# Kernel tuning notes

Hardware: AMD Instinct MI355X
Metric: run time of the kernel (lower is better)

The kernel has to match this reference:

```python
import jax, jax.numpy as jnp
import numpy as np

C = 64
SHIFT = 3
NEIGHBOR_SIZES = (3, 5, 7)  # dilation = 1 for all levels
NUM_GROUPS = 8


def conv2d(x, w, b, padding=0, groups=1):
    out = jax.lax.conv_general_dilated(
        x, w, (1, 1), [(padding, padding), (padding, padding)],
        dimension_numbers=('NCHW', 'OIHW', 'NCHW'),
        feature_group_count=groups)
    return out + b[None, :, None, None]


def natten_level(q, k, v, rpb, ks):
    # q,k,v: (B,H,W,C) channels-last; rpb: (2ks-1, 2ks-1); dilation=1.
    # NATTEN semantics: window of size ks x ks centered at each query, clamped
    # (shifted) at image borders so it always lies fully inside the image.
    B, H, W, Cc = q.shape
    r = ks // 2
    i = jnp.arange(H); ni = jnp.clip(i - r, 0, H - ks)   # window row starts
    j = jnp.arange(W); nj = jnp.clip(j - r, 0, W - ks)   # window col starts
    ar = jnp.arange(ks)
    ii = ni[:, None] + ar[None, :]                        # (H,ks) neighbor rows
    jj = nj[:, None] + ar[None, :]                        # (W,ks) neighbor cols
    kn = k[:, ii][:, :, :, jj]                            # (B,H,ks,W,ks,C)
    attn = jnp.einsum('bhwc,bhpwqc->bhwpq', q, kn)        # (B,H,W,ks,ks)
    # relative-position-bias lookup: row start pi = (ks-1) + ni - i
    pi = (ks - 1) + ni - i                                # (H,)
    pj = (ks - 1) + nj - j                                # (W,)
    bias = rpb[(pi[:, None] + ar[None, :])[:, None, :, None],
               (pj[:, None] + ar[None, :])[None, :, None, :]]  # (H,W,ks,ks)
    attn = attn + bias[None]
    attn = jax.nn.softmax(attn.reshape(B, H, W, ks * ks), axis=-1)
    attn = attn.reshape(B, H, W, ks, ks)
    vn = v[:, ii][:, :, :, jj]                            # (B,H,ks,W,ks,C)
    return jnp.einsum('bhwpq,bhpwqc->bhwc', attn, vn)


def _forward(sup_frame, key_frame, conv_smooth_w, conv_smooth_b,
             conv_reduce_w, conv_reduce_b, v_w0, v_b0, v_w1, v_b1,
             v_w2, v_b2, rpb0, rpb1, rpb2, fusion_w, fusion_b):
    p = SHIFT
    outs = [sup_frame]  # original (pre-shift) support features
    # shift-roll spatial correlation
    shifts = [(sh, sw) for sh in (-p, 0, p) for sw in (-p, 0, p)
              if not (sh == 0 and sw == 0)]
    padded = jnp.pad(sup_frame, ((0, 0), (0, 0), (p, p), (p, p)))
    parts = jnp.split(padded, NUM_GROUPS, axis=1)
    shifted = jnp.concatenate(
        [jnp.roll(parts[g], shifts[g], axis=(2, 3)) for g in range(NUM_GROUPS)],
        axis=1)[..., p:-p, p:-p]
    shifted = conv2d(shifted, conv_smooth_w, conv_smooth_b, padding=1,
                     groups=NUM_GROUPS)
    sup2 = conv2d(jnp.concatenate([sup_frame, shifted], axis=1),
                  conv_reduce_w, conv_reduce_b)
    # multi-scale neighborhood attention (single head)
    q = jnp.transpose(key_frame, (0, 2, 3, 1))
    k = jnp.transpose(sup2, (0, 2, 3, 1))
    v_ws = (v_w0, v_w1, v_w2); v_bs = (v_b0, v_b1, v_b2)
    rpbs = (rpb0, rpb1, rpb2)
    for lvl, ks in enumerate(NEIGHBOR_SIZES):
        v = jnp.transpose(conv2d(sup2, v_ws[lvl], v_bs[lvl]), (0, 2, 3, 1))
        agg = natten_level(q, k, v, rpbs[lvl], ks)
        outs.append(jnp.transpose(agg, (0, 3, 1, 2)))
    fused = jnp.concatenate(outs, axis=1)  # (B, 4*C, H, W)
    return jax.nn.relu(conv2d(fused, fusion_w, fusion_b, padding=1))


def setup_inputs() -> dict:
    key = jax.random.key(0)
    ks = jax.random.split(key, 20)
    B, H, W = 4, 96, 96
    s = 0.05
    d = {}
    d['sup_frame'] = jax.random.normal(ks[0], (B, C, H, W), jnp.float32)
    d['key_frame'] = jax.random.normal(ks[1], (B, C, H, W), jnp.float32)
    d['conv_smooth_w'] = jax.random.normal(ks[2], (C, C // NUM_GROUPS, 3, 3), jnp.float32) * s
    d['conv_smooth_b'] = jnp.zeros((C,), jnp.float32)
    d['conv_reduce_w'] = jax.random.normal(ks[3], (C, 2 * C, 1, 1), jnp.float32) * s
    d['conv_reduce_b'] = jnp.zeros((C,), jnp.float32)
    for i, nk in enumerate(NEIGHBOR_SIZES):
        d[f'v_w{i}'] = jax.random.normal(ks[4 + i], (C, C, 1, 1), jnp.float32) * s
        d[f'v_b{i}'] = jnp.zeros((C,), jnp.float32)
        d[f'rpb{i}'] = jax.random.normal(ks[8 + i], (2 * nk - 1, 2 * nk - 1), jnp.float32) * 0.02
    d['fusion_w'] = jax.random.normal(ks[12], (C, C * (len(NEIGHBOR_SIZES) + 1), 3, 3), jnp.float32) * s
    d['fusion_b'] = jnp.zeros((C,), jnp.float32)
    return d


def reference(sup_frame, key_frame, conv_smooth_w, conv_smooth_b,
              conv_reduce_w, conv_reduce_b, v_w0, v_b0, v_w1, v_b1,
              v_w2, v_b2, rpb0, rpb1, rpb2, fusion_w, fusion_b):
    return _forward(sup_frame, key_frame, conv_smooth_w, conv_smooth_b,
                    conv_reduce_w, conv_reduce_b, v_w0, v_b0, v_w1, v_b1,
                    v_w2, v_b2, rpb0, rpb1, rpb2, fusion_w, fusion_b)
```

## Files before the change

kernel.cpp:

```cpp
#include <hip/hip_runtime.h>
#include <hip/hip_bf16.h>

#define HW 9216
#define NPX 36864

typedef __attribute__((ext_vector_type(8))) short short8;
typedef __attribute__((ext_vector_type(4))) float f32x4;

static __device__ __forceinline__ unsigned short f2bf(float x) {
    union { __hip_bfloat16 h; unsigned short u; } c; c.h = __float2bfloat16(x); return c.u;
}
static __device__ __forceinline__ float bfl(unsigned int u){ return __uint_as_float(u << 16); }
static __device__ __forceinline__ float bfh(unsigned int u){ return __uint_as_float(u & 0xffff0000u); }

__global__ __launch_bounds__(256) void prep_weights(
    const float* __restrict__ rw, const float* __restrict__ vw0,
    const float* __restrict__ vw1, const float* __restrict__ vw2,
    const float* __restrict__ fw,
    float* __restrict__ rwT, unsigned short* __restrict__ vwF, unsigned short* __restrict__ fwF)
{
    int idx = blockIdx.x * 256 + threadIdx.x;
    if (idx < 8192) {
        int c = idx & 63, i = idx >> 6;
        rwT[idx] = rw[c * 128 + i];
    } else if (idx < 20480) {
        int e = idx - 8192;
        int j = e & 7, lane = (e >> 3) & 63, kf = (e >> 9) & 1, nt = (e >> 10) & 3, lvl = e >> 12;
        int co = nt * 16 + (lane & 15);
        int k = kf * 32 + (lane >> 4) * 8 + j;
        const float* vw = (lvl == 0) ? vw0 : ((lvl == 1) ? vw1 : vw2);
        vwF[e] = f2bf(vw[co * 64 + k]);
    } else if (idx < 167936) {
        int e = idx - 20480;
        int j = e & 7, lane = (e >> 3) & 63, nt = (e >> 9) & 3, kc = e >> 11;
        int co = nt * 16 + (lane & 15);
        int k = kc * 32 + ((lane >> 4) << 3) + j;
        int tap = k >> 8, ci = k & 255;
        fwF[e] = f2bf(fw[co * 2304 + ci * 9 + tap]);
    }
}

__global__ void pack_kernel(const float* __restrict__ key, const float* __restrict__ sup,
                            float* __restrict__ qT, __hip_bfloat16* __restrict__ fused)
{
    __shared__ float lk[32][33], ls[32][33];
    int tx = threadIdx.x, ty = threadIdx.y;
    int x0 = blockIdx.x * 32, c0 = blockIdx.y * 32;
    int z = blockIdx.z; int b = z / 96, y = z - b * 96;
    #pragma unroll
    for (int i = 0; i < 32; i += 8) {
        int c = c0 + ty + i;
        lk[ty + i][tx] = key[((b * 64 + c) * 96 + y) * 96 + x0 + tx];
        ls[ty + i][tx] = sup[((b * 64 + c) * 96 + y) * 96 + x0 + tx];
    }
    __syncthreads();
    #pragma unroll
    for (int i = 0; i < 32; i += 8) {
        int px = (b * 96 + y) * 96 + x0 + ty + i;
        qT[px * 64 + c0 + tx]     = lk[tx][ty + i];
        fused[px * 256 + c0 + tx] = __hip_bfloat16(ls[tx][ty + i]);
    }
}

__global__ __launch_bounds__(256) void shift_smooth(const float* __restrict__ sup,
    const float* __restrict__ w, const float* __restrict__ bias, float* __restrict__ smooth)
{
    __shared__ __align__(16) float tile[8][34][36];
    int bid = blockIdx.x;
    int half = bid & 1;
    int sj   = (bid >> 1) % 9;
    int grp  = (bid / 18) & 7;
    int b    = bid / 144;
    int sby = sj / 3, sbx = sj % 3;
    int Y0 = sby * 32, X0 = sbx * 32;
    int sh = 3 * ((grp >= 5) - (grp < 3));
    int mm = (grp < 3) ? grp : ((grp < 5) ? ((grp == 3) ? 0 : 2) : (grp - 5));
    int sw = 3 * mm - 3;
    int t = threadIdx.x;

    const float* supg = sup + (size_t)(b * 64 + grp * 8) * HW;
    #pragma unroll
    for (int pp = 0; pp < 5; pp++) {
        int pos = pp * 256 + t;
        if (pos < 1156) {
            int r = pos / 34, u = pos - r * 34;
            int yy = Y0 - 1 + r, xx = X0 - 1 + u;
            int ys = yy - sh, xs = xx - sw;
            bool ok = (yy >= 0) & (yy < 96) & (xx >= 0) & (xx < 96) &
                      (ys >= 0) & (ys < 96) & (xs >= 0) & (xs < 96);
            int addr = ok ? (ys * 96 + xs) : 0;
            #pragma unroll
            for (int ic = 0; ic < 8; ic++) {
                float v = supg[(size_t)ic * HW + addr];
                tile[ic][r][u] = ok ? v : 0.f;
            }
        }
    }
    __syncthreads();

    int c = __builtin_amdgcn_readfirstlane(grp * 8 + half * 4 + (t >> 6));
    int lane = t & 63;
    int ty4 = lane >> 3, tx4 = lane & 7;
    int py0 = ty4 * 4, x0r = tx4 * 4;

    float bz = bias[c];
    float acc[4][4];
    #pragma unroll
    for (int jr = 0; jr < 4; jr++)
        #pragma unroll
        for (int j = 0; j < 4; j++) acc[jr][j] = bz;

    const float* wp = w + c * 72;
    for (int ic = 0; ic < 8; ic++) {
        float wr[9];
        #pragma unroll
        for (int q = 0; q < 9; q++) wr[q] = wp[ic * 9 + q];
        #pragma unroll
        for (int rr = 0; rr < 6; rr++) {
            float4 fa = *(const float4*)&tile[ic][py0 + rr][x0r];
            float4 fb4 = *(const float4*)&tile[ic][py0 + rr][x0r + 4];
            float f[6] = {fa.x, fa.y, fa.z, fa.w, fb4.x, fb4.y};
            #pragma unroll
            for (int ky = 0; ky < 3; ky++) {
                int jr = rr - ky;
                if (jr >= 0 && jr < 4) {
                    #pragma unroll
                    for (int j = 0; j < 4; j++)
                        acc[jr][j] += wr[ky*3]*f[j] + wr[ky*3+1]*f[j+1] + wr[ky*3+2]*f[j+2];
                }
            }
        }
    }

    float* op = smooth + ((size_t)(b * 64 + c) * 96 + Y0 + py0) * 96 + X0 + x0r;
    #pragma unroll
    for (int jr = 0; jr < 4; jr++) {
        float4 st = {acc[jr][0], acc[jr][1], acc[jr][2], acc[jr][3]};
        *(float4*)(op + (size_t)jr * 96) = st;
    }
}

__global__ __launch_bounds__(256) void reduce_kernel(const float* __restrict__ sup,
    const float* __restrict__ smooth, const float* __restrict__ rwT,
    const float* __restrict__ rb, float* __restrict__ sup2)
{
    __shared__ __align__(16) float wlds[8192];
    int t = threadIdx.x;
    #pragma unroll
    for (int e = 0; e < 8; e++) {
        int idx = (e * 256 + t) * 4;
        *(float4*)&wlds[idx] = *(const float4*)&rwT[idx];
    }
    __syncthreads();

    int lane = t & 63, wq = t >> 6;
    int px = blockIdx.x * 64 + lane;
    int b = px / HW; int rem = px - b * HW;
    const float* s1 = sup + (size_t)b * 64 * HW + rem;
    const float* s2 = smooth + (size_t)b * 64 * HW + rem;
    float acc[16];
    #pragma unroll
    for (int j = 0; j < 16; j++) acc[j] = rb[wq * 16 + j];

    #pragma unroll 8
    for (int i = 0; i < 64; i++) {
        float v = s1[i * HW];
        const float* wr = &wlds[i * 64 + wq * 16];
        float4 w0 = *(const float4*)wr, w1 = *(const float4*)(wr + 4);
        float4 w2 = *(const float4*)(wr + 8), w3 = *(const float4*)(wr + 12);
        acc[0] += w0.x * v;  acc[1] += w0.y * v;  acc[2] += w0.z * v;  acc[3] += w0.w * v;
        acc[4] += w1.x * v;  acc[5] += w1.y * v;  acc[6] += w1.z * v;  acc[7] += w1.w * v;
        acc[8] += w2.x * v;  acc[9] += w2.y * v;  acc[10] += w2.z * v; acc[11] += w2.w * v;
        acc[12] += w3.x * v; acc[13] += w3.y * v; acc[14] += w3.z * v; acc[15] += w3.w * v;
    }
    #pragma unroll 8
    for (int i = 0; i < 64; i++) {
        float v = s2[i * HW];
        const float* wr = &wlds[(64 + i) * 64 + wq * 16];
        float4 w0 = *(const float4*)wr, w1 = *(const float4*)(wr + 4);
        float4 w2 = *(const float4*)(wr + 8), w3 = *(const float4*)(wr + 12);
        acc[0] += w0.x * v;  acc[1] += w0.y * v;  acc[2] += w0.z * v;  acc[3] += w0.w * v;
        acc[4] += w1.x * v;  acc[5] += w1.y * v;  acc[6] += w1.z * v;  acc[7] += w1.w * v;
        acc[8] += w2.x * v;  acc[9] += w2.y * v;  acc[10] += w2.z * v; acc[11] += w2.w * v;
        acc[12] += w3.x * v; acc[13] += w3.y * v; acc[14] += w3.z * v; acc[15] += w3.w * v;
    }

    float* op = sup2 + (size_t)px * 64 + wq * 16;
    #pragma unroll
    for (int j = 0; j < 16; j += 4) { float4 st = {acc[j], acc[j+1], acc[j+2], acc[j+3]}; *(float4*)(op + j) = st; }
}

template<int KS>
__device__ __forceinline__ void level_softmax(int qc, int y, int x, int ni7, int nj7,
        const float* __restrict__ rpb, const float* dots_row, float* out_row)
{
    constexpr int R = KS / 2, KK = KS * KS, NB = 2 * KS - 1;
    constexpr int NE = (KK + 3) / 4;
    int ni = min(max(y - R, 0), 96 - KS), nj = min(max(x - R, 0), 96 - KS);
    int di = ni - ni7, dj = nj - nj7;
    int br = KS - 1 + ni - y, bc = KS - 1 + nj - x;
    float sv[NE];
    float mx = -1e30f;
    #pragma unroll
    for (int i = 0; i < NE; i++) {
        int e = qc + i * 4;
        if (e < KK) {
            int ey = e / KS, ex = e - ey * KS;
            float s = dots_row[(di + ey) * 7 + dj + ex] + rpb[(br + ey) * NB + bc + ex];
            sv[i] = s; mx = fmaxf(mx, s);
        } else sv[i] = -1e30f;
    }
    mx = fmaxf(mx, __shfl_xor(mx, 1)); mx = fmaxf(mx, __shfl_xor(mx, 2));
    float sum = 0.f;
    #pragma unroll
    for (int i = 0; i < NE; i++) { sv[i] = __expf(sv[i] - mx); sum += sv[i]; }
    sum += __shfl_xor(sum, 1); sum += __shfl_xor(sum, 2);
    float inv = 1.f / sum;
    #pragma unroll
    for (int i = 0; i < NE; i++) {
        int e = qc + i * 4;
        if (e < KK) out_row[e] = sv[i] * inv;
    }
}

__global__ __launch_bounds__(256) void natten_fused(
    const float* __restrict__ qT, const float* __restrict__ sup2,
    const unsigned short* __restrict__ vwF,
    const float* __restrict__ vb0, const float* __restrict__ vb1, const float* __restrict__ vb2,
    const float* __restrict__ rpb0, const float* __restrict__ rpb1, const float* __restrict__ rpb2,
    __hip_bfloat16* __restrict__ fused)
{
    __shared__ __align__(16) unsigned short khalo[196 * 72];
    __shared__ float dots[64][50];
    __shared__ float a3[64][12];
    __shared__ float a5[64][28];

    int t = threadIdx.x;
    int bb = blockIdx.y;
    int tx0 = (blockIdx.x % 12) * 8, ty0 = (blockIdx.x / 12) * 8;
    const float* kb = sup2 + (size_t)bb * HW * 64;

    for (int it = 0; it < 13; it++) {
        int qidx = it * 256 + t;
        if (qidx < 3136) {
            int cq = qidx & 15, pos = qidx >> 4;
            int py = pos / 14, pxx = pos - py * 14;
            int gy = min(max(ty0 - 3 + py, 0), 95);
            int gx = min(max(tx0 - 3 + pxx, 0), 95);
            float4 v = *(const float4*)(kb + (((size_t)gy * 96 + gx) << 6) + cq * 4);
            ushort4 pk = {f2bf(v.x), f2bf(v.y), f2bf(v.z), f2bf(v.w)};
            *(ushort4*)&khalo[pos * 72 + cq * 4] = pk;
        }
    }
    __syncthreads();

    int pxl = t >> 2, qc = t & 3;
    int pty = pxl >> 3, ptx = pxl & 7;
    int y = ty0 + pty, x = tx0 + ptx;
    int gpx = bb * HW + y * 96 + x;

    float qv[16];
    {
        const float* qp = qT + (size_t)gpx * 64 + qc * 16;
        #pragma unroll
        for (int j = 0; j < 16; j += 4) {
            float4 q4 = *(const float4*)(qp + j);
            qv[j] = q4.x; qv[j+1] = q4.y; qv[j+2] = q4.z; qv[j+3] = q4.w;
        }
    }

    int ni7 = min(max(y - 3, 0), 89), nj7 = min(max(x - 3, 0), 89);
    int ly = ni7 - (ty0 - 3), lx = nj7 - (tx0 - 3);

    for (int oy = 0; oy < 7; oy++) {
        #pragma unroll
        for (int ox = 0; ox < 7; ox++) {
            const unsigned short* kp = &khalo[((ly + oy) * 14 + lx + ox) * 72 + qc * 16];
            uint4 ka = *(const uint4*)kp;
            uint4 kc = *(const uint4*)(kp + 8);
            float d = qv[0]*bfl(ka.x) + qv[1]*bfh(ka.x) + qv[2]*bfl(ka.y) + qv[3]*bfh(ka.y)
                    + qv[4]*bfl(ka.z) + qv[5]*bfh(ka.z) + qv[6]*bfl(ka.w) + qv[7]*bfh(ka.w)
                    + qv[8]*bfl(kc.x) + qv[9]*bfh(kc.x) + qv[10]*bfl(kc.y) + qv[11]*bfh(kc.y)
                    + qv[12]*bfl(kc.z) + qv[13]*bfh(kc.z) + qv[14]*bfl(kc.w) + qv[15]*bfh(kc.w);
            d += __shfl_xor(d, 1);
            d += __shfl_xor(d, 2);
            if (qc == 0) dots[pxl][oy * 7 + ox] = d;
        }
    }

    level_softmax<3>(qc, y, x, ni7, nj7, rpb0, &dots[pxl][0], &a3[pxl][0]);
    level_softmax<5>(qc, y, x, ni7, nj7, rpb1, &dots[pxl][0], &a5[pxl][0]);
    level_softmax<7>(qc, y, x, ni7, nj7, rpb2, &dots[pxl][0], &dots[pxl][0]);

    int ni5 = min(max(y - 2, 0), 91), nj5 = min(max(x - 2, 0), 91);
    int ni3 = min(max(y - 1, 0), 93), nj3 = min(max(x - 1, 0), 93);
    int di5 = ni5 - ni7, dj5 = nj5 - nj7, di3 = ni3 - ni7, dj3 = nj3 - nj7;

    float s2[3][16];
    #pragma unroll
    for (int l = 0; l < 3; l++)
        #pragma unroll
        for (int j = 0; j < 16; j++) s2[l][j] = 0.f;

    for (int oy = 0; oy < 7; oy++) {
        #pragma unroll
        for (int ox = 0; ox < 7; ox++) {
            const unsigned short* kp = &khalo[((ly + oy) * 14 + lx + ox) * 72 + qc * 16];
            uint4 ka = *(const uint4*)kp;
            uint4 kc = *(const uint4*)(kp + 8);
            float kv[16] = {bfl(ka.x), bfh(ka.x), bfl(ka.y), bfh(ka.y),
                            bfl(ka.z), bfh(ka.z), bfl(ka.w), bfh(ka.w),
                            bfl(kc.x), bfh(kc.x), bfl(kc.y), bfh(kc.y),
                            bfl(kc.z), bfh(kc.z), bfl(kc.w), bfh(kc.w)};
            float w7 = dots[pxl][oy * 7 + ox];
            #pragma unroll
            for (int j = 0; j < 16; j++) s2[2][j] += w7 * kv[j];
            int e5y = oy - di5, e5x = ox - dj5;
            if ((unsigned)e5y < 5u && (unsigned)e5x < 5u) {
                float w5 = a5[pxl][e5y * 5 + e5x];
                #pragma unroll
                for (int j = 0; j < 16; j++) s2[1][j] += w5 * kv[j];
            }
            int e3y = oy - di3, e3x = ox - dj3;
            if ((unsigned)e3y < 3u && (unsigned)e3x < 3u) {
                float w3 = a3[pxl][e3y * 3 + e3x];
                #pragma unroll
                for (int j = 0; j < 16; j++) s2[0][j] += w3 * kv[j];
            }
        }
    }
    __syncthreads();

    unsigned short* sproj = khalo;
    #pragma unroll
    for (int l = 0; l < 3; l++) {
        unsigned int pk[8];
        #pragma unroll
        for (int j = 0; j < 8; j++)
            pk[j] = (unsigned int)f2bf(s2[l][2*j]) | ((unsigned int)f2bf(s2[l][2*j+1]) << 16);
        unsigned int* dst = (unsigned int*)&sproj[(l * 64 + pxl) * 72 + qc * 16];
        uint4 s0 = {pk[0], pk[1], pk[2], pk[3]};
        uint4 s1 = {pk[4], pk[5], pk[6], pk[7]};
        *(uint4*)dst = s0;
        *(uint4*)(dst + 4) = s1;
    }
    __syncthreads();

    int wv = t >> 6, lane = t & 63;
    int lm = lane & 15, quad = lane >> 4;
    #pragma unroll
    for (int l = 0; l < 3; l++) {
        f32x4 acc[4];
        #pragma unroll
        for (int nt = 0; nt < 4; nt++) acc[nt] = (f32x4){0.f, 0.f, 0.f, 0.f};
        #pragma unroll
        for (int kf = 0; kf < 2; kf++) {
            short8 a = *(const short8*)&sproj[(l * 64 + wv * 16 + lm) * 72 + kf * 32 + quad * 8];
            #pragma unroll
            for (int nt = 0; nt < 4; nt++) {
                short8 bfr = *(const short8*)&vwF[(((l * 4 + nt) * 2 + kf) * 64 + lane) * 8];
                acc[nt] = __builtin_amdgcn_mfma_f32_16x16x32_bf16(a, bfr, acc[nt], 0, 0, 0);
            }
        }
        const float* vbl = (l == 0) ? vb0 : ((l == 1) ? vb1 : vb2);
        #pragma unroll
        for (int nt = 0; nt < 4; nt++)
            #pragma unroll
            for (int r = 0; r < 4; r++) {
                int p = wv * 16 + quad * 4 + r;
                int co = nt * 16 + lm;
                int py = p >> 3, pxx = p & 7;
                size_t off = ((size_t)(bb * HW + (ty0 + py) * 96 + tx0 + pxx) << 8) + (l + 1) * 64 + co;
                fused[off] = __hip_bfloat16(acc[nt][r] + vbl[co]);
            }
    }
}

__global__ __launch_bounds__(256) void fusion_mfma(
    const __hip_bfloat16* __restrict__ fB, const unsigned short* __restrict__ fwF,
    const float* __restrict__ fb, float* __restrict__ out)
{
    __shared__ __align__(16) unsigned short ah[108 * 72];
    __shared__ float lds_out[64 * 66];
    int t = threadIdx.x;
    int wv = t >> 6, lane = t & 63, lm = lane & 15, quad = lane >> 4;
    int X0 = blockIdx.x * 16, Y0 = blockIdx.y * 4, b = blockIdx.z;
    const unsigned short* fBu = (const unsigned short*)fB;

    f32x4 acc[4] = {};

    for (int chunk = 0; chunk < 4; chunk++) {
        __syncthreads();
        #pragma unroll
        for (int ee = 0; ee < 4; ee++) {
            int e = ee * 256 + t;
            if (e < 864) {
                int seg = e & 7, hp = e >> 3;
                int hy = hp / 18, hx = hp - hy * 18;
                int gy = Y0 - 1 + hy, gx = X0 - 1 + hx;
                bool ok = (gy >= 0) & (gy < 96) & (gx >= 0) & (gx < 96);
                short8 v = {};
                if (ok) v = *(const short8*)(fBu + (((size_t)(b * HW + gy * 96 + gx)) << 8) + chunk * 64 + seg * 8);
                *(short8*)&ah[hp * 72 + seg * 8] = v;
            }
        }
        __syncthreads();
        #pragma unroll
        for (int ky = 0; ky < 3; ky++) {
            #pragma unroll
            for (int kx = 0; kx < 3; kx++) {
                #pragma unroll
                for (int kf = 0; kf < 2; kf++) {
                    short8 a = *(const short8*)&ah[((wv + ky) * 18 + lm + kx) * 72 + kf * 32 + quad * 8];
                    int kc = (ky * 3 + kx) * 8 + chunk * 2 + kf;
                    const unsigned short* bp = fwF + ((size_t)(kc * 4) * 64 + lane) * 8;
                    acc[0] = __builtin_amdgcn_mfma_f32_16x16x32_bf16(a, *(const short8*)(bp),        acc[0], 0, 0, 0);
                    acc[1] = __builtin_amdgcn_mfma_f32_16x16x32_bf16(a, *(const short8*)(bp + 512),  acc[1], 0, 0, 0);
                    acc[2] = __builtin_amdgcn_mfma_f32_16x16x32_bf16(a, *(const short8*)(bp + 1024), acc[2], 0, 0, 0);
                    acc[3] = __builtin_amdgcn_mfma_f32_16x16x32_bf16(a, *(const short8*)(bp + 1536), acc[3], 0, 0, 0);
                }
            }
        }
    }

    #pragma unroll
    for (int nt = 0; nt < 4; nt++)
        #pragma unroll
        for (int r = 0; r < 4; r++) {
            int p = wv * 16 + quad * 4 + r;
            int co = nt * 16 + lm;
            lds_out[co * 66 + p] = acc[nt][r];
        }
    __syncthreads();

    int p2 = t & 63, py = p2 >> 4, px2 = p2 & 15;
    float* ob = out + ((size_t)(b * 64) * 96 + Y0 + py) * 96 + X0 + px2;
    #pragma unroll 4
    for (int i = 0; i < 16; i++) {
        int co = (t >> 6) * 16 + i;
        float v = lds_out[co * 66 + p2] + fb[co];
        ob[(size_t)co * HW] = v > 0.f ? v : 0.f;
    }
}

extern "C" void kernel_launch(void* const* d_in, const int* in_sizes, int n_in,
                              void* d_out, int out_size, void* d_ws, size_t ws_size,
                              hipStream_t stream) {
    const float* sup = (const float*)d_in[0];
    const float* key = (const float*)d_in[1];
    const float* smw = (const float*)d_in[2];
    const float* smb = (const float*)d_in[3];
    const float* rw  = (const float*)d_in[4];
    const float* rb  = (const float*)d_in[5];
    const float *vw[3], *vb[3], *rpb[3];
    if (in_sizes[8] == 25) {
        for (int l = 0; l < 3; l++) {
            vw[l]  = (const float*)d_in[6 + 3 * l];
            vb[l]  = (const float*)d_in[7 + 3 * l];
            rpb[l] = (const float*)d_in[8 + 3 * l];
        }
    } else {
        for (int l = 0; l < 3; l++) {
            vw[l]  = (const float*)d_in[6 + 2 * l];
            vb[l]  = (const float*)d_in[7 + 2 * l];
            rpb[l] = (const float*)d_in[12 + l];
        }
    }
    const float* fw = (const float*)d_in[15];
    const float* fb = (const float*)d_in[16];
    float* out = (float*)d_out;

    float* wsf    = (float*)d_ws;
    float* smooth = wsf;
    float* sup2   = wsf + 2359296;
    float* qT     = wsf + 4718592;
    float* rwT    = wsf + 7077888;
    unsigned short* vwF = (unsigned short*)(wsf + 7086080);
    __hip_bfloat16* fusedB = (__hip_bfloat16*)(wsf + 7092224);
    unsigned short* fwF    = (unsigned short*)(wsf + 11810816);

    prep_weights<<<dim3(656), dim3(256), 0, stream>>>(rw, vw[0], vw[1], vw[2], fw, rwT, vwF, fwF);
    pack_kernel<<<dim3(3, 2, 384), dim3(32, 8), 0, stream>>>(key, sup, qT, fusedB);
    shift_smooth<<<dim3(576), dim3(256), 0, stream>>>(sup, smw, smb, smooth);
    reduce_kernel<<<dim3(576), dim3(256), 0, stream>>>(sup, smooth, rwT, rb, sup2);
    natten_fused<<<dim3(144, 4), dim3(256), 0, stream>>>(qT, sup2, vwF,
        vb[0], vb[1], vb[2], rpb[0], rpb[1], rpb[2], fusedB);
    fusion_mfma<<<dim3(6, 24, 4), dim3(256), 0, stream>>>(fusedB, fwF, fb, out);
}
```

Baseline: 224.7 us.

## Shrink natten LDS with fp16 scores, stage rpb in LDS, remap lanes

```diff
diff --git a/kernel.cpp b/kernel.cpp
--- a/kernel.cpp
+++ b/kernel.cpp
@@ -192,7 +192,7 @@
 
 template<int KS>
 __device__ __forceinline__ void level_softmax(int qc, int y, int x, int ni7, int nj7,
-        const float* __restrict__ rpb, const float* dots_row, float* out_row)
+        const _Float16* rpbl, const _Float16* dots_row, _Float16* out_row)
 {
     constexpr int R = KS / 2, KK = KS * KS, NB = 2 * KS - 1;
     constexpr int NE = (KK + 3) / 4;
@@ -206,24 +206,24 @@
         int e = qc + i * 4;
         if (e < KK) {
             int ey = e / KS, ex = e - ey * KS;
-            float s = dots_row[(di + ey) * 7 + dj + ex] + rpb[(br + ey) * NB + bc + ex];
+            float s = (float)dots_row[(di + ey) * 7 + dj + ex] + (float)rpbl[(br + ey) * NB + bc + ex];
             sv[i] = s; mx = fmaxf(mx, s);
         } else sv[i] = -1e30f;
     }
-    mx = fmaxf(mx, __shfl_xor(mx, 1)); mx = fmaxf(mx, __shfl_xor(mx, 2));
+    mx = fmaxf(mx, __shfl_xor(mx, 16)); mx = fmaxf(mx, __shfl_xor(mx, 32));
     float sum = 0.f;
     #pragma unroll
     for (int i = 0; i < NE; i++) { sv[i] = __expf(sv[i] - mx); sum += sv[i]; }
-    sum += __shfl_xor(sum, 1); sum += __shfl_xor(sum, 2);
+    sum += __shfl_xor(sum, 16); sum += __shfl_xor(sum, 32);
     float inv = 1.f / sum;
     #pragma unroll
     for (int i = 0; i < NE; i++) {
         int e = qc + i * 4;
-        if (e < KK) out_row[e] = sv[i] * inv;
-    }
-}
-
-__global__ __launch_bounds__(256) void natten_fused(
+        if (e < KK) out_row[e] = (_Float16)(sv[i] * inv);
+    }
+}
+
+__global__ __launch_bounds__(256, 4) void natten_fused(
     const float* __restrict__ qT, const float* __restrict__ sup2,
     const unsigned short* __restrict__ vwF,
     const float* __restrict__ vb0, const float* __restrict__ vb1, const float* __restrict__ vb2,
@@ -231,14 +231,20 @@
     __hip_bfloat16* __restrict__ fused)
 {
     __shared__ __align__(16) unsigned short khalo[196 * 72];
-    __shared__ float dots[64][50];
-    __shared__ float a3[64][12];
-    __shared__ float a5[64][28];
+    __shared__ _Float16 dots[64][52];
+    __shared__ _Float16 a3[64][12];
+    __shared__ _Float16 a5[64][28];
+    __shared__ _Float16 rlds[276];
 
     int t = threadIdx.x;
     int bb = blockIdx.y;
     int tx0 = (blockIdx.x % 12) * 8, ty0 = (blockIdx.x / 12) * 8;
     const float* kb = sup2 + (size_t)bb * HW * 64;
+
+    for (int e = t; e < 275; e += 256) {
+        float v = (e < 169) ? rpb2[e] : ((e < 250) ? rpb1[e - 169] : rpb0[e - 250]);
+        rlds[e] = (_Float16)v;
+    }
 
     for (int it = 0; it < 13; it++) {
         int qidx = it * 256 + t;
@@ -254,7 +260,9 @@
     }
     __syncthreads();
 
-    int pxl = t >> 2, qc = t & 3;
+    int lane = t & 63, wv = t >> 6;
+    int pxl = wv * 16 + (lane & 15);
+    int qc = lane >> 4;
     int pty = pxl >> 3, ptx = pxl & 7;
     int y = ty0 + pty, x = tx0 + ptx;
     int gpx = bb * HW + y * 96 + x;
@@ -278,19 +286,20 @@
             const unsigned short* kp = &khalo[((ly + oy) * 14 + lx + ox) * 72 + qc * 16];
             uint4 ka = *(const uint4*)kp;
             uint4 kc = *(const uint4*)(kp + 8);
-            float d = qv[0]*bfl(ka.x) + qv[1]*bfh(ka.x) + qv[2]*bfl(ka.y) + qv[3]*bfh(ka.y)
-                    + qv[4]*bfl(ka.z) + qv[5]*bfh(ka.z) + qv[6]*bfl(ka.w) + qv[7]*bfh(ka.w)
-                    + qv[8]*bfl(kc.x) + qv[9]*bfh(kc.x) + qv[10]*bfl(kc.y) + qv[11]*bfh(kc.y)
-                    + qv[12]*bfl(kc.z) + qv[13]*bfh(kc.z) + qv[14]*bfl(kc.w) + qv[15]*bfh(kc.w);
-            d += __shfl_xor(d, 1);
-            d += __shfl_xor(d, 2);
-            if (qc == 0) dots[pxl][oy * 7 + ox] = d;
-        }
-    }
-
-    level_softmax<3>(qc, y, x, ni7, nj7, rpb0, &dots[pxl][0], &a3[pxl][0]);
-    level_softmax<5>(qc, y, x, ni7, nj7, rpb1, &dots[pxl][0], &a5[pxl][0]);
-    level_softmax<7>(qc, y, x, ni7, nj7, rpb2, &dots[pxl][0], &dots[pxl][0]);
+            float p0 = qv[0]*bfl(ka.x) + qv[1]*bfh(ka.x) + qv[2]*bfl(ka.y) + qv[3]*bfh(ka.y);
+            float p1 = qv[4]*bfl(ka.z) + qv[5]*bfh(ka.z) + qv[6]*bfl(ka.w) + qv[7]*bfh(ka.w);
+            float p2 = qv[8]*bfl(kc.x) + qv[9]*bfh(kc.x) + qv[10]*bfl(kc.y) + qv[11]*bfh(kc.y);
+            float p3 = qv[12]*bfl(kc.z) + qv[13]*bfh(kc.z) + qv[14]*bfl(kc.w) + qv[15]*bfh(kc.w);
+            float d = (p0 + p1) + (p2 + p3);
+            d += __shfl_xor(d, 16);
+            d += __shfl_xor(d, 32);
+            if (qc == 0) dots[pxl][oy * 7 + ox] = (_Float16)d;
+        }
+    }
+
+    level_softmax<3>(qc, y, x, ni7, nj7, rlds + 250, &dots[pxl][0], &a3[pxl][0]);
+    level_softmax<5>(qc, y, x, ni7, nj7, rlds + 169, &dots[pxl][0], &a5[pxl][0]);
+    level_softmax<7>(qc, y, x, ni7, nj7, rlds,       &dots[pxl][0], &dots[pxl][0]);
 
     int ni5 = min(max(y - 2, 0), 91), nj5 = min(max(x - 2, 0), 91);
     int ni3 = min(max(y - 1, 0), 93), nj3 = min(max(x - 1, 0), 93);
@@ -312,18 +321,18 @@
                             bfl(ka.z), bfh(ka.z), bfl(ka.w), bfh(ka.w),
                             bfl(kc.x), bfh(kc.x), bfl(kc.y), bfh(kc.y),
                             bfl(kc.z), bfh(kc.z), bfl(kc.w), bfh(kc.w)};
-            float w7 = dots[pxl][oy * 7 + ox];
+            float w7 = (float)dots[pxl][oy * 7 + ox];
             #pragma unroll
             for (int j = 0; j < 16; j++) s2[2][j] += w7 * kv[j];
             int e5y = oy - di5, e5x = ox - dj5;
             if ((unsigned)e5y < 5u && (unsigned)e5x < 5u) {
-                float w5 = a5[pxl][e5y * 5 + e5x];
+                float w5 = (float)a5[pxl][e5y * 5 + e5x];
                 #pragma unroll
                 for (int j = 0; j < 16; j++) s2[1][j] += w5 * kv[j];
             }
             int e3y = oy - di3, e3x = ox - dj3;
             if ((unsigned)e3y < 3u && (unsigned)e3x < 3u) {
-                float w3 = a3[pxl][e3y * 3 + e3x];
+                float w3 = (float)a3[pxl][e3y * 3 + e3x];
                 #pragma unroll
                 for (int j = 0; j < 16; j++) s2[0][j] += w3 * kv[j];
             }
@@ -346,7 +355,6 @@
     }
     __syncthreads();
 
-    int wv = t >> 6, lane = t & 63;
     int lm = lane & 15, quad = lane >> 4;
     #pragma unroll
     for (int l = 0; l < 3; l++) {
```

Result: slower. 341.4 us (+51.9%).
